# Kernel optimization log

Hardware: AMD Instinct MI355X
Metric: run time of the kernel (lower is better)

The kernel has to match this reference:

```python
import jax, jax.numpy as jnp
import numpy as np
import math

IN_CH, OUT_CH, RANK, MODES, HEAD, BATCH = 64, 64, 8, 8192, 4, 32


def setup_inputs() -> dict:
    key = jax.random.key(0)
    kx, k1, k2, k3 = jax.random.split(key, 4)
    scale = 1.0 / math.sqrt(IN_CH * OUT_CH)
    x = jax.random.normal(kx, (BATCH, IN_CH, MODES), dtype=jnp.float32)
    # Note: in the torch module, self.U1 has in_channels rows and is used as the
    # FIRST contraction ('irkh'), while self.U2 has out_channels rows and is the
    # LAST ('oskh') — the jit'd function's arg names are swapped relative to the
    # module attributes. We name params by their role here.
    U_in = scale * jax.random.uniform(k1, (IN_CH, RANK, MODES, HEAD), dtype=jnp.float32)   # self.U1
    M = scale * jax.random.uniform(k2, (RANK, RANK, MODES, HEAD), dtype=jnp.float32)       # self.M
    U_out = scale * jax.random.uniform(k3, (OUT_CH, RANK, MODES, HEAD), dtype=jnp.float32) # self.U2
    return {"x": x, "U_in": U_in, "M": M, "U_out": U_out}


def reference(x, U_in, M, U_out):
    # x: [b, i, k] -> r: [b, r, k, h]
    r = jnp.einsum('irkh,bik->brkh', U_in, x)
    # mix ranks per (mode, head): [b, s, k, h]
    s = jnp.einsum('rskh,brkh->bskh', M, r)
    # project to out channels, sum over heads: [b, o, k]
    out = jnp.einsum('oskh,bskh->bok', U_out, s)
    return out
```

## Files before the change

kernel.cpp:

```cpp
#include <hip/hip_runtime.h>


static constexpr int IN_CH  = 64;
static constexpr int OUT_CH = 64;
static constexpr int RANK   = 8;
static constexpr int MODES  = 8192;
static constexpr int KT     = 16;
static constexpr int CROWS  = 64;
static constexpr int CF4    = CROWS * KT;

typedef const __attribute__((address_space(1))) void* gas_t;
typedef __attribute__((address_space(3))) void* las_t;

__device__ __forceinline__ void fma_s4(float4& a, const float4 w, const float v) {
    a.x = fmaf(w.x, v, a.x); a.y = fmaf(w.y, v, a.y);
    a.z = fmaf(w.z, v, a.z); a.w = fmaf(w.w, v, a.w);
}
__device__ __forceinline__ void fma_44(float4& a, const float4 w, const float4 v) {
    a.x = fmaf(w.x, v.x, a.x); a.y = fmaf(w.y, v.y, a.y);
    a.z = fmaf(w.z, v.z, a.z); a.w = fmaf(w.w, v.w, a.w);
}

__device__ __forceinline__ void stage_chunk(const float4* gbase, float4* lbuf,
                                            int wid, int lane) {
    const int sub = lane >> 4;
    const int col = lane & 15;
#pragma unroll
    for (int j = 0; j < 4; ++j) {
        const int row0 = wid * 16 + j * 4;
        const float4* src = gbase + (size_t)(row0 + sub) * MODES + col;
        float4* dst = lbuf + row0 * KT;
        __builtin_amdgcn_global_load_lds((gas_t)src, (las_t)dst, 16, 0, 0);
    }
}

__global__ __launch_bounds__(256, 2) void diag_lr_fused(
    const float*  __restrict__ x,
    const float4* __restrict__ Uin,
    const float4* __restrict__ Mw,
    const float4* __restrict__ Uout,
    float*        __restrict__ out)
{
    __shared__ float4 lds[2][CF4];

    const int t    = threadIdx.x;
    const int kk   = t & 15;
    const int bs   = t >> 4;
    const int lane = t & 63;
    const int wid  = t >> 6;
    const int k0   = blockIdx.x * KT;
    const int k    = k0 + kk;

    const float4* UinB = Uin  + k0;
    const float4* MB   = Mw   + k0;
    const float4* UoB  = Uout + k0;
    const float*  xp0 = x + (size_t)bs        * (IN_CH * MODES) + k;
    const float*  xp1 = x + (size_t)(bs + 16) * (IN_CH * MODES) + k;
    float*        op0 = out + (size_t)bs        * (OUT_CH * MODES) + k;
    float*        op1 = out + (size_t)(bs + 16) * (OUT_CH * MODES) + k;

    stage_chunk(UinB, &lds[0][0], wid, lane);
    float xa[2][2][8];
#pragma unroll
    for (int ii = 0; ii < 8; ++ii) {
        xa[0][0][ii] = xp0[ii * MODES];
        xa[0][1][ii] = xp1[ii * MODES];
    }

    float4 r0[RANK], r1[RANK];
#pragma unroll
    for (int r = 0; r < RANK; ++r) {
        r0[r] = make_float4(0.f, 0.f, 0.f, 0.f);
        r1[r] = make_float4(0.f, 0.f, 0.f, 0.f);
    }

#pragma unroll
    for (int c = 0; c < 8; ++c) {
        const int buf = c & 1;
        const float4* nxt = (c < 7) ? (UinB + (size_t)(c + 1) * CROWS * MODES) : MB;
        stage_chunk(nxt, &lds[buf ^ 1][0], wid, lane);
        if (c < 7) {
#pragma unroll
            for (int ii = 0; ii < 8; ++ii) {
                xa[buf ^ 1][0][ii] = xp0[((c + 1) * 8 + ii) * MODES];
                xa[buf ^ 1][1][ii] = xp1[((c + 1) * 8 + ii) * MODES];
            }
        }
        if (c < 7) asm volatile("s_waitcnt vmcnt(20)" ::: "memory");
        else       asm volatile("s_waitcnt vmcnt(4)"  ::: "memory");
        __builtin_amdgcn_s_barrier();
        asm volatile("" ::: "memory");
        const float4* Lb = &lds[buf][0];
#pragma unroll
        for (int ii = 0; ii < 8; ++ii) {
            const float xv0 = xa[buf][0][ii];
            const float xv1 = xa[buf][1][ii];
#pragma unroll
            for (int r = 0; r < RANK; ++r) {
                const float4 w = Lb[(ii * 8 + r) * KT + kk];
                fma_s4(r0[r], w, xv0);
                fma_s4(r1[r], w, xv1);
            }
        }
        asm volatile("" ::: "memory");
        __builtin_amdgcn_s_barrier();
    }

    float4 s0[RANK], s1[RANK];
#pragma unroll
    for (int s = 0; s < RANK; ++s) {
        s0[s] = make_float4(0.f, 0.f, 0.f, 0.f);
        s1[s] = make_float4(0.f, 0.f, 0.f, 0.f);
    }
    {
        stage_chunk(UoB, &lds[1][0], wid, lane);
        asm volatile("s_waitcnt vmcnt(4)" ::: "memory");
        __builtin_amdgcn_s_barrier();
        asm volatile("" ::: "memory");
        const float4* Lb = &lds[0][0];
#pragma unroll
        for (int r = 0; r < RANK; ++r)
#pragma unroll
            for (int s = 0; s < RANK; ++s) {
                const float4 w = Lb[(r * 8 + s) * KT + kk];
                fma_44(s0[s], w, r0[r]);
                fma_44(s1[s], w, r1[r]);
            }
        asm volatile("" ::: "memory");
        __builtin_amdgcn_s_barrier();
    }

#pragma unroll
    for (int c = 0; c < 8; ++c) {
        const int buf = (c + 1) & 1;
        if (c < 7) {
            stage_chunk(UoB + (size_t)(c + 1) * CROWS * MODES, &lds[buf ^ 1][0], wid, lane);
            asm volatile("s_waitcnt vmcnt(4)" ::: "memory");
        } else {
            asm volatile("s_waitcnt vmcnt(0)" ::: "memory");
        }
        __builtin_amdgcn_s_barrier();
        asm volatile("" ::: "memory");
        const float4* Lb = &lds[buf][0];
#pragma unroll
        for (int oo = 0; oo < 8; ++oo) {
            float4 a0 = make_float4(0.f, 0.f, 0.f, 0.f);
            float4 a1 = make_float4(0.f, 0.f, 0.f, 0.f);
#pragma unroll
            for (int s = 0; s < RANK; ++s) {
                const float4 w = Lb[(oo * 8 + s) * KT + kk];
                fma_44(a0, w, s0[s]);
                fma_44(a1, w, s1[s]);
            }
            op0[(c * 8 + oo) * MODES] = (a0.x + a0.y) + (a0.z + a0.w);
            op1[(c * 8 + oo) * MODES] = (a1.x + a1.y) + (a1.z + a1.w);
        }
        if (c < 7) {
            asm volatile("" ::: "memory");
            __builtin_amdgcn_s_barrier();
        }
    }
}

extern "C" void kernel_launch(void* const* d_in, const int* in_sizes, int n_in,
                              void* d_out, int out_size, void* d_ws, size_t ws_size,
                              hipStream_t stream) {
    const float*  x    = (const float*)d_in[0];
    const float4* Uin  = (const float4*)d_in[1];
    const float4* Mw   = (const float4*)d_in[2];
    const float4* Uout = (const float4*)d_in[3];
    float* out = (float*)d_out;

    dim3 grid(512), block(256);
    hipLaunchKernelGGL(diag_lr_fused, grid, block, 0, stream, x, Uin, Mw, Uout, out);
}
```

Baseline: 82.75 us.

## Deepen LDS staging to a four-buffer ring with prefetch distance two

Replaces the double-buffered LDS staging with a four-slot ring that runs as one continuous chunk sequence across all three contraction phases (U_in, M, U_out). Each chunk is now issued two steps ahead, and the trailing barrier after each compute step is removed, leaving one barrier per chunk. The aim is to keep more global-to-LDS loads in flight and cut synchronisation stalls in this bandwidth-bound kernel. In exchange, LDS per block doubles to 64 KB, which could limit occupancy, and correctness now depends on the hand-tuned vmcnt wait counts.

Measured after the change: 83.21 us. Within noise of the previous version (+0.6%).

```diff
diff --git a/kernel.cpp b/kernel.cpp
--- a/kernel.cpp
+++ b/kernel.cpp
@@ -41,7 +41,7 @@
     const float4* __restrict__ Uout,
     float*        __restrict__ out)
 {
-    __shared__ float4 lds[2][CF4];
+    __shared__ float4 lds[4][CF4];
 
     const int t    = threadIdx.x;
     const int kk   = t & 15;
@@ -59,13 +59,20 @@
     float*        op0 = out + (size_t)bs        * (OUT_CH * MODES) + k;
     float*        op1 = out + (size_t)(bs + 16) * (OUT_CH * MODES) + k;
 
-    stage_chunk(UinB, &lds[0][0], wid, lane);
+    auto chunk_ptr = [&](int c) -> const float4* {
+        return (c < 8)  ? (UinB + (size_t)c * CROWS * MODES)
+             : (c == 8) ? MB
+                        : (UoB + (size_t)(c - 9) * CROWS * MODES);
+    };
+
     float xa[2][2][8];
 #pragma unroll
     for (int ii = 0; ii < 8; ++ii) {
         xa[0][0][ii] = xp0[ii * MODES];
         xa[0][1][ii] = xp1[ii * MODES];
     }
+    stage_chunk(chunk_ptr(0), &lds[0][0], wid, lane);
+    stage_chunk(chunk_ptr(1), &lds[1][0], wid, lane);
 
     float4 r0[RANK], r1[RANK];
 #pragma unroll
@@ -76,25 +83,24 @@
 
 #pragma unroll
     for (int c = 0; c < 8; ++c) {
-        const int buf = c & 1;
-        const float4* nxt = (c < 7) ? (UinB + (size_t)(c + 1) * CROWS * MODES) : MB;
-        stage_chunk(nxt, &lds[buf ^ 1][0], wid, lane);
+        asm volatile("" ::: "memory");
         if (c < 7) {
 #pragma unroll
             for (int ii = 0; ii < 8; ++ii) {
-                xa[buf ^ 1][0][ii] = xp0[((c + 1) * 8 + ii) * MODES];
-                xa[buf ^ 1][1][ii] = xp1[((c + 1) * 8 + ii) * MODES];
+                xa[(c + 1) & 1][0][ii] = xp0[((c + 1) * 8 + ii) * MODES];
+                xa[(c + 1) & 1][1][ii] = xp1[((c + 1) * 8 + ii) * MODES];
             }
         }
-        if (c < 7) asm volatile("s_waitcnt vmcnt(20)" ::: "memory");
-        else       asm volatile("s_waitcnt vmcnt(4)"  ::: "memory");
+        stage_chunk(chunk_ptr(c + 2), &lds[(c + 2) & 3][0], wid, lane);
+        if (c <= 6) asm volatile("s_waitcnt vmcnt(24)" ::: "memory");
+        else        asm volatile("s_waitcnt vmcnt(8)"  ::: "memory");
         __builtin_amdgcn_s_barrier();
         asm volatile("" ::: "memory");
-        const float4* Lb = &lds[buf][0];
+        const float4* Lb = &lds[c & 3][0];
 #pragma unroll
         for (int ii = 0; ii < 8; ++ii) {
-            const float xv0 = xa[buf][0][ii];
-            const float xv1 = xa[buf][1][ii];
+            const float xv0 = xa[c & 1][0][ii];
+            const float xv1 = xa[c & 1][1][ii];
 #pragma unroll
             for (int r = 0; r < RANK; ++r) {
                 const float4 w = Lb[(ii * 8 + r) * KT + kk];
@@ -102,8 +108,6 @@
                 fma_s4(r1[r], w, xv1);
             }
         }
-        asm volatile("" ::: "memory");
-        __builtin_amdgcn_s_barrier();
     }
 
     float4 s0[RANK], s1[RANK];
@@ -113,11 +117,12 @@
         s1[s] = make_float4(0.f, 0.f, 0.f, 0.f);
     }
     {
-        stage_chunk(UoB, &lds[1][0], wid, lane);
-        asm volatile("s_waitcnt vmcnt(4)" ::: "memory");
+        asm volatile("" ::: "memory");
+        stage_chunk(chunk_ptr(10), &lds[10 & 3][0], wid, lane);
+        asm volatile("s_waitcnt vmcnt(8)" ::: "memory");
         __builtin_amdgcn_s_barrier();
         asm volatile("" ::: "memory");
-        const float4* Lb = &lds[0][0];
+        const float4* Lb = &lds[8 & 3][0];
 #pragma unroll
         for (int r = 0; r < RANK; ++r)
 #pragma unroll
@@ -126,22 +131,18 @@
                 fma_44(s0[s], w, r0[r]);
                 fma_44(s1[s], w, r1[r]);
             }
-        asm volatile("" ::: "memory");
-        __builtin_amdgcn_s_barrier();
     }
 
 #pragma unroll
-    for (int c = 0; c < 8; ++c) {
-        const int buf = (c + 1) & 1;
-        if (c < 7) {
-            stage_chunk(UoB + (size_t)(c + 1) * CROWS * MODES, &lds[buf ^ 1][0], wid, lane);
-            asm volatile("s_waitcnt vmcnt(4)" ::: "memory");
-        } else {
-            asm volatile("s_waitcnt vmcnt(0)" ::: "memory");
-        }
+    for (int c = 9; c < 17; ++c) {
+        asm volatile("" ::: "memory");
+        if (c + 2 <= 16)
+            stage_chunk(chunk_ptr(c + 2), &lds[(c + 2) & 3][0], wid, lane);
+        asm volatile("s_waitcnt vmcnt(8)" ::: "memory");
         __builtin_amdgcn_s_barrier();
         asm volatile("" ::: "memory");
-        const float4* Lb = &lds[buf][0];
+        const float4* Lb = &lds[c & 3][0];
+        const int oc = c - 9;
 #pragma unroll
         for (int oo = 0; oo < 8; ++oo) {
             float4 a0 = make_float4(0.f, 0.f, 0.f, 0.f);
@@ -152,12 +153,8 @@
                 fma_44(a0, w, s0[s]);
                 fma_44(a1, w, s1[s]);
             }
-            op0[(c * 8 + oo) * MODES] = (a0.x + a0.y) + (a0.z + a0.w);
-            op1[(c * 8 + oo) * MODES] = (a1.x + a1.y) + (a1.z + a1.w);
-        }
-        if (c < 7) {
-            asm volatile("" ::: "memory");
-            __builtin_amdgcn_s_barrier();
+            op0[(oc * 8 + oo) * MODES] = (a0.x + a0.y) + (a0.z + a0.w);
+            op1[(oc * 8 + oo) * MODES] = (a1.x + a1.y) + (a1.z + a1.w);
         }
     }
 }
```
